# Kernel tuning notes

Measured on AMD Instinct MI355X. Metric: run time of the kernel, lower is better.

The kernel has to match this reference:

```python
import jax, jax.numpy as jnp
import numpy as np

B, S, E, H = 4, 2048, 1024, 16
K = 9           # number of boundaries per batch (K-1 = 8 passages)
DH = E // H


def make_relevance_mask(boundaries, relevance_scores, seq_len):
    """Vectorized equivalent of the Python-loop mask builder.

    boundaries: (B, K) int, sorted; boundaries[:,0] == q_end.
    relevance_scores: (B, K-1) float.
    Returns float mask (B, S, S) with values {0, 1, relevance}.
    """
    Bsz, Kb = boundaries.shape
    idx = jnp.arange(seq_len, dtype=boundaries.dtype)
    # pid[b, s] = j s.t. boundaries[b, j] <= s < boundaries[b, j+1]; -1 before b[0]
    pid = jax.vmap(lambda bb: jnp.searchsorted(bb, idx, side='right'))(boundaries) - 1  # (B,S)
    in_pass = (pid >= 0) & (pid < Kb - 1)  # inside some passage span
    rel_g = jnp.take_along_axis(relevance_scores, jnp.clip(pid, 0, Kb - 2), axis=1)  # (B,S)
    # query rows (pos < q_end): columns in passage j -> relevance[j], else 1
    col_val = jnp.where(in_pass, rel_g, 1.0)  # (B,S)
    qrow = idx[None, :] < boundaries[:, :1]   # (B,S)
    # non-query rows: 1 iff same passage block, else 0
    same = in_pass[:, :, None] & in_pass[:, None, :] & (pid[:, :, None] == pid[:, None, :])
    mask = jnp.where(qrow[:, :, None], col_val[:, None, :], jnp.where(same, 1.0, 0.0))
    return mask.astype(jnp.float32)


def setup_inputs() -> dict:
    key = jax.random.key(0)
    k1, k2, k3, k4, k5, k6, k7 = jax.random.split(key, 7)
    hidden_states = jax.random.normal(k1, (B, S, E), dtype=jnp.float32)
    relevance_scores = jax.random.uniform(k2, (B, K - 1), dtype=jnp.float32)
    passage_boundaries = jnp.sort(jax.random.randint(k3, (B, K), 0, S, dtype=jnp.int32), axis=1)
    in_proj_w = 0.02 * jax.random.normal(k4, (3 * E, E), dtype=jnp.float32)
    in_proj_b = jnp.zeros((3 * E,), dtype=jnp.float32)
    out_w = 0.02 * jax.random.normal(k5, (E, E), dtype=jnp.float32)
    out_b = jnp.zeros((E,), dtype=jnp.float32)
    return {
        'hidden_states': hidden_states,
        'relevance_scores': relevance_scores,
        'passage_boundaries': passage_boundaries,
        'in_proj_w': in_proj_w,
        'in_proj_b': in_proj_b,
        'out_w': out_w,
        'out_b': out_b,
    }


def reference(hidden_states, relevance_scores, passage_boundaries,
              in_proj_w, in_proj_b, out_w, out_b):
    Bsz, Sl, Em = hidden_states.shape
    mask = make_relevance_mask(passage_boundaries, relevance_scores, Sl)  # (B,S,S)
    qkv = hidden_states @ in_proj_w.T + in_proj_b              # (B,S,3E)
    q, k, v = jnp.split(qkv, 3, axis=-1)
    def heads(t):
        return t.reshape(Bsz, Sl, H, DH).transpose(0, 2, 1, 3)  # (B,H,S,Dh)
    q, k, v = heads(q), heads(k), heads(v)
    scale = 1.0 / jnp.sqrt(jnp.float32(DH))
    scores = jnp.einsum('bhqd,bhkd->bhqk', q * scale, k) + mask[:, None]  # float mask is ADDED
    attn = jax.nn.softmax(scores, axis=-1)
    out = jnp.einsum('bhqk,bhkd->bhqd', attn, v)
    out = out.transpose(0, 2, 1, 3).reshape(Bsz, Sl, Em)
    return out @ out_w.T + out_b
```

## Files before the change

kernel.cpp:

```cpp
#include <hip/hip_runtime.h>
#include <math.h>

#define Bsz 4
#define Sq  2048
#define Eq  1024
#define Hh  16
#define DHd 64
#define Kb  9
#define LOG2E 1.44269504088896340736f
#define NCLS 10

typedef _Float16 f16;
typedef __attribute__((ext_vector_type(8))) _Float16 fh8;
typedef __attribute__((ext_vector_type(4))) _Float16 fh4;
typedef __attribute__((ext_vector_type(2))) _Float16 fh2;
typedef __attribute__((ext_vector_type(4))) float fx4;
typedef __attribute__((ext_vector_type(16))) float fx16;
typedef __attribute__((ext_vector_type(4))) int i4;

#define SWZ(r, c) ((r) * 64 + ((c) ^ (((r) & 7) << 3)))

static __device__ __forceinline__ float fexp2(float x) {
#if __has_builtin(__builtin_amdgcn_exp2f)
  return __builtin_amdgcn_exp2f(x);
#else
  return __expf(x * 0.6931471805599453f);
#endif
}

__global__ void pid_kernel(const int* __restrict__ bnd, const float* __restrict__ rel,
                           int* __restrict__ pidr, float* __restrict__ lfTab) {
  int idx = blockIdx.x * blockDim.x + threadIdx.x;
  if (idx >= Bsz * Sq) return;
  int b = idx >> 11;
  int s = idx & (Sq - 1);
  int j = -1;
#pragma unroll
  for (int t = 0; t < Kb; ++t) {
    if (bnd[b * Kb + t] <= s) j = t;
  }
  pidr[idx] = j;
  bool inp = (j >= 0 && j < Kb - 1);
  float cv = inp ? rel[b * (Kb - 1) + j] : 1.0f;
  float* base = &lfTab[(size_t)b * NCLS * Sq + s];
  base[0] = cv * LOG2E;
#pragma unroll
  for (int c = 1; c < NCLS; ++c)
    base[c * Sq] = (inp && j == c - 1) ? LOG2E : 0.0f;
}

__global__ __launch_bounds__(256) void cvt_hs(const float* __restrict__ x,
                                              f16* __restrict__ xo) {
  int i = (blockIdx.x * blockDim.x + threadIdx.x) * 8;
  float4 a = *(const float4*)&x[i];
  float4 b = *(const float4*)&x[i + 4];
  fh8 o;
  o[0] = (f16)a.x; o[1] = (f16)a.y; o[2] = (f16)a.z; o[3] = (f16)a.w;
  o[4] = (f16)b.x; o[5] = (f16)b.y; o[6] = (f16)b.z; o[7] = (f16)b.w;
  *(fh8*)&xo[i] = o;
}

template <int MODE>
__global__ __launch_bounds__(256) void gemm_f16(
    const f16* __restrict__ A, const f16* __restrict__ Bh,
    const float* __restrict__ bias, float* __restrict__ Cp,
    int M, int N, int Kd,
    f16* __restrict__ qo, f16* __restrict__ ko, f16* __restrict__ vto) {
  __shared__ __align__(16) f16 Ash[2][128 * 64];
  __shared__ __align__(16) f16 Bsh[2][128 * 64];

  const int tid = threadIdx.x;
  const int lane = tid & 63, w = tid >> 6;
  const int wm = w >> 1, wn = w & 1;
  const int q16 = lane & 15, quad = lane >> 4;
  const int m_blk = blockIdx.y * 128, n_blk = blockIdx.x * 128;

  fx4 acc[4][4];
#pragma unroll
  for (int mt = 0; mt < 4; ++mt)
#pragma unroll
    for (int nt = 0; nt < 4; ++nt)
#pragma unroll
      for (int r = 0; r < 4; ++r) acc[mt][nt][r] = 0.f;

  const int rl = lane >> 3;
  const int bc = ((lane & 7) * 8) ^ (rl << 3);
  const f16* gA = A + (size_t)m_blk * Kd;
  const f16* gB = Bh + (size_t)n_blk * Kd;

  auto stage = [&](f16* dstA, f16* dstB, int k0) {
#pragma unroll
    for (int j = 0; j < 4; ++j) {
      const int r = w * 32 + j * 8;
      const f16* pa = gA + (size_t)(r + rl) * Kd + k0 + bc;
      const f16* pb = gB + (size_t)(r + rl) * Kd + k0 + bc;
#if __has_builtin(__builtin_amdgcn_global_load_lds)
      __builtin_amdgcn_global_load_lds(
          (const __attribute__((address_space(1))) void*)pa,
          (__attribute__((address_space(3))) void*)(dstA + r * 64), 16, 0, 0);
      __builtin_amdgcn_global_load_lds(
          (const __attribute__((address_space(1))) void*)pb,
          (__attribute__((address_space(3))) void*)(dstB + r * 64), 16, 0, 0);
#else
      *(fh8*)&dstA[r * 64 + lane * 8] = *(const fh8*)pa;
      *(fh8*)&dstB[r * 64 + lane * 8] = *(const fh8*)pb;
#endif
    }
  };

  stage(Ash[0], Bsh[0], 0);
  __syncthreads();

  for (int k0 = 0; k0 < Kd; k0 += 64) {
    const int c = (k0 >> 6) & 1;
    if (k0 + 64 < Kd) stage(Ash[c ^ 1], Bsh[c ^ 1], k0 + 64);

#pragma unroll
    for (int ks = 0; ks < 2; ++ks) {
      fh8 af[4], bfr[4];
#pragma unroll
      for (int mt = 0; mt < 4; ++mt)
        af[mt] = *(const fh8*)&Ash[c][SWZ(wm * 64 + mt * 16 + q16, ks * 32 + quad * 8)];
#pragma unroll
      for (int nt = 0; nt < 4; ++nt)
        bfr[nt] = *(const fh8*)&Bsh[c][SWZ(wn * 64 + nt * 16 + q16, ks * 32 + quad * 8)];
#pragma unroll
      for (int nt = 0; nt < 4; ++nt)
#pragma unroll
        for (int mt = 0; mt < 4; ++mt)
          acc[mt][nt] = __builtin_amdgcn_mfma_f32_16x16x32_f16(af[mt], bfr[nt], acc[mt][nt], 0, 0, 0);
    }
    __syncthreads();
  }

  float bsv[4];
#pragma unroll
  for (int nt = 0; nt < 4; ++nt) bsv[nt] = bias[n_blk + wn * 64 + nt * 16 + q16];

  if (MODE == 0) {
#pragma unroll
    for (int mt = 0; mt < 4; ++mt)
#pragma unroll
      for (int r = 0; r < 4; ++r) {
        int row = m_blk + wm * 64 + mt * 16 + quad * 4 + r;
#pragma unroll
        for (int nt = 0; nt < 4; ++nt) {
          int col = n_blk + wn * 64 + nt * 16 + q16;
          Cp[(size_t)row * N + col] = acc[mt][nt][r] + bsv[nt];
        }
      }
  } else {
    const int n0 = n_blk + wn * 64;
    const int which = n0 >> 10;
    const int hd = (n0 & 1023) >> 6;
    const float scale = (which == 0) ? 0.125f * LOG2E : 1.0f;
#pragma unroll
    for (int mt = 0; mt < 4; ++mt)
#pragma unroll
      for (int r = 0; r < 4; ++r) {
        int m = m_blk + wm * 64 + mt * 16 + quad * 4 + r;
        int b = m >> 11, s = m & (Sq - 1);
#pragma unroll
        for (int nt = 0; nt < 4; ++nt) {
          int d = nt * 16 + q16;
          float x = (acc[mt][nt][r] + bsv[nt]) * scale;
          if (which == 2) {
            vto[(((size_t)(b * Hh + hd)) * DHd + d) * Sq + s] = (f16)x;
          } else {
            f16* dst = (which == 0) ? qo : ko;
            dst[(((size_t)(b * Hh + hd)) * Sq + s) * DHd + d] = (f16)x;
          }
        }
      }
  }
}

__global__ __launch_bounds__(256, 2) void attn_v6(
    const f16* __restrict__ Qf, const f16* __restrict__ Kf,
    const f16* __restrict__ Vt, const int* __restrict__ pidr,
    const float* __restrict__ lfTab, f16* __restrict__ attf) {
  const int lin = blockIdx.x;
  const int orig = (lin & 7) * 128 + (lin >> 3);
  const int qb = orig & 15, hd = (orig >> 4) & 15, b = orig >> 8;
  const int bh = b * Hh + hd;
  const int tid = threadIdx.x;
  const int lane = tid & 63, w = tid >> 6;
  const int l31 = lane & 31, hi = lane >> 5;

  __shared__ __align__(16) f16 Ks[2][64 * 64];
  __shared__ __align__(16) f16 Vs[2][64 * 64];

  const size_t qkbase = (size_t)bh * Sq * DHd;
  const size_t vtbase = (size_t)bh * DHd * Sq;
  const int qrow = qb * 128 + w * 32 + l31;

  fh8 qf[4];
  {
    const f16* qp = &Qf[qkbase + (size_t)qrow * DHd + hi * 8];
#pragma unroll
    for (int ds = 0; ds < 4; ++ds) qf[ds] = *(const fh8*)&qp[ds * 16];
  }

  const int rq = pidr[b * Sq + qrow];
  const float* lfrow = &lfTab[((size_t)(b * NCLS + (rq + 1))) * Sq + 4 * hi];

  fh8 onesf;
#pragma unroll
  for (int j = 0; j < 8; ++j) onesf[j] = (l31 == 0) ? (f16)1.0f : (f16)0.0f;

  fx16 o_acc[2], lacc;
#pragma unroll
  for (int r = 0; r < 16; ++r) { o_acc[0][r] = 0.f; o_acc[1][r] = 0.f; lacc[r] = 0.f; }

  const int sr = tid >> 2, sc = (tid & 3) * 16;
  const int NT = Sq / 64;

  fh8 kc0, kc1, vc0, vc1;
  {
    const f16* gk = &Kf[qkbase + (size_t)sr * DHd + sc];
    kc0 = *(const fh8*)&gk[0]; kc1 = *(const fh8*)&gk[8];
    const f16* gv = &Vt[vtbase + (size_t)sr * Sq + sc];
    vc0 = *(const fh8*)&gv[0]; vc1 = *(const fh8*)&gv[8];
  }
  *(fh8*)&Ks[0][SWZ(sr, sc)]     = kc0;
  *(fh8*)&Ks[0][SWZ(sr, sc + 8)] = kc1;
  *(fh8*)&Vs[0][SWZ(sr, sc)]     = vc0;
  *(fh8*)&Vs[0][SWZ(sr, sc + 8)] = vc1;
  {
    const f16* gk = &Kf[qkbase + (size_t)(64 + sr) * DHd + sc];
    kc0 = *(const fh8*)&gk[0]; kc1 = *(const fh8*)&gk[8];
    const f16* gv = &Vt[vtbase + (size_t)sr * Sq + 64 + sc];
    vc0 = *(const fh8*)&gv[0]; vc1 = *(const fh8*)&gv[8];
  }
  __syncthreads();

  fx16 sacc0, sacc1;

  for (int kt = 0; kt < NT; ++kt) {
    const int c = kt & 1;

    {
      const float* lp = &lfrow[kt * 64];
#pragma unroll
      for (int g = 0; g < 4; ++g) {
        float4 a = *(const float4*)&lp[8 * g];
        sacc0[4 * g + 0] = a.x; sacc0[4 * g + 1] = a.y;
        sacc0[4 * g + 2] = a.z; sacc0[4 * g + 3] = a.w;
      }
    }

    if (kt + 1 < NT) {
      *(fh8*)&Ks[c ^ 1][SWZ(sr, sc)]     = kc0;
      *(fh8*)&Ks[c ^ 1][SWZ(sr, sc + 8)] = kc1;
      *(fh8*)&Vs[c ^ 1][SWZ(sr, sc)]     = vc0;
      *(fh8*)&Vs[c ^ 1][SWZ(sr, sc + 8)] = vc1;
      if (kt + 2 < NT) {
        const f16* gk = &Kf[qkbase + (size_t)((kt + 2) * 64 + sr) * DHd + sc];
        kc0 = *(const fh8*)&gk[0]; kc1 = *(const fh8*)&gk[8];
        const f16* gv = &Vt[vtbase + (size_t)sr * Sq + (kt + 2) * 64 + sc];
        vc0 = *(const fh8*)&gv[0]; vc1 = *(const fh8*)&gv[8];
      }
    }

    auto half = [&](fx16& sacc, int s, bool preload_next) {
      fh8 kfr[4];
#pragma unroll
      for (int ds = 0; ds < 4; ++ds)
        kfr[ds] = *(const fh8*)&Ks[c][SWZ(s * 32 + l31, ds * 16 + hi * 8)];
      __builtin_amdgcn_s_setprio(1);
#pragma unroll
      for (int ds = 0; ds < 4; ++ds)
        sacc = __builtin_amdgcn_mfma_f32_32x32x16_f16(kfr[ds], qf[ds], sacc, 0, 0, 0);
      __builtin_amdgcn_s_setprio(0);

      if (preload_next) {
        const float* lp = &lfrow[kt * 64 + 32];
#pragma unroll
        for (int g = 0; g < 4; ++g) {
          float4 a = *(const float4*)&lp[8 * g];
          sacc1[4 * g + 0] = a.x; sacc1[4 * g + 1] = a.y;
          sacc1[4 * g + 2] = a.z; sacc1[4 * g + 3] = a.w;
        }
      }

      int pk[8];
#pragma unroll
      for (int i = 0; i < 8; ++i) {
        fh2 h;
        h[0] = (f16)fexp2(sacc[2 * i]);
        h[1] = (f16)fexp2(sacc[2 * i + 1]);
        pk[i] = __builtin_bit_cast(int, h);
      }

      fh8 vfr[2][2];
#pragma unroll
      for (int dt = 0; dt < 2; ++dt)
#pragma unroll
        for (int kb = 0; kb < 2; ++kb)
          vfr[dt][kb] = *(const fh8*)&Vs[c][SWZ(dt * 32 + l31, s * 32 + kb * 16 + hi * 8)];

      __builtin_amdgcn_s_setprio(1);
#pragma unroll
      for (int kb = 0; kb < 2; ++kb) {
        int a01 = pk[4 * kb + 0], a23 = pk[4 * kb + 1];
        int a45 = pk[4 * kb + 2], a67 = pk[4 * kb + 3];
        i4 t;
#if __has_builtin(__builtin_amdgcn_permlane32_swap)
        auto s0 = __builtin_amdgcn_permlane32_swap(a01, a45, false, false);
        auto s1 = __builtin_amdgcn_permlane32_swap(a23, a67, false, false);
        t[0] = s0[0]; t[1] = s1[0]; t[2] = s0[1]; t[3] = s1[1];
#else
        int x01 = __shfl_xor(a01, 32), x23 = __shfl_xor(a23, 32);
        int x45 = __shfl_xor(a45, 32), x67 = __shfl_xor(a67, 32);
        t[0] = hi ? x45 : a01; t[1] = hi ? x67 : a23;
        t[2] = hi ? a45 : x01; t[3] = hi ? a67 : x23;
#endif
        fh8 pf = __builtin_bit_cast(fh8, t);
        lacc = __builtin_amdgcn_mfma_f32_32x32x16_f16(onesf, pf, lacc, 0, 0, 0);
        o_acc[0] = __builtin_amdgcn_mfma_f32_32x32x16_f16(vfr[0][kb], pf, o_acc[0], 0, 0, 0);
        o_acc[1] = __builtin_amdgcn_mfma_f32_32x32x16_f16(vfr[1][kb], pf, o_acc[1], 0, 0, 0);
      }
      __builtin_amdgcn_s_setprio(0);
    };

    half(sacc0, 0, true);
    half(sacc1, 1, false);

    if (kt + 1 < NT) __syncthreads();
  }

  float l = __shfl(lacc[0], l31);
  float inv = 1.0f / l;
  size_t obase = ((size_t)(b * Sq + qrow)) * Eq + hd * 64 + 4 * hi;
#pragma unroll
  for (int dt = 0; dt < 2; ++dt)
#pragma unroll
    for (int g = 0; g < 4; ++g) {
      fh4 o4;
#pragma unroll
      for (int j = 0; j < 4; ++j) o4[j] = (f16)(o_acc[dt][4 * g + j] * inv);
      *(fh4*)&attf[obase + dt * 32 + 8 * g] = o4;
    }
}

extern "C" void kernel_launch(void* const* d_in, const int* in_sizes, int n_in,
                              void* d_out, int out_size, void* d_ws, size_t ws_size,
                              hipStream_t stream) {
  const float* hs = (const float*)d_in[0];
  const float* rel = (const float*)d_in[1];
  const int* bnd = (const int*)d_in[2];
  const float* wi = (const float*)d_in[3];
  const float* bi = (const float*)d_in[4];
  const float* wo = (const float*)d_in[5];
  const float* bo = (const float*)d_in[6];
  float* out = (float*)d_out;

  const size_t NQ = (size_t)Bsz * Hh * Sq * DHd;
  char* p = (char*)d_ws;
  f16* qf = (f16*)p;   p += NQ * 2;
  f16* kf = (f16*)p;   p += NQ * 2;
  f16* vt = (f16*)p;   p += NQ * 2;
  f16* hsf = (f16*)p;  p += NQ * 2;
  f16* attf = (f16*)p; p += NQ * 2;
  f16* wif = (f16*)p;  p += (size_t)3 * Eq * Eq * 2;
  f16* wof = (f16*)p;  p += (size_t)Eq * Eq * 2;
  int* pidr = (int*)p; p += Bsz * Sq * 4;
  float* lfTab = (float*)p;

  hipLaunchKernelGGL(pid_kernel, dim3((Bsz * Sq + 255) / 256), dim3(256), 0, stream,
                     bnd, rel, pidr, lfTab);
  hipLaunchKernelGGL(cvt_hs, dim3((int)(NQ / 2048)), dim3(256), 0, stream, hs, hsf);
  hipLaunchKernelGGL(cvt_hs, dim3(3 * Eq * Eq / 2048), dim3(256), 0, stream, wi, wif);
  hipLaunchKernelGGL(cvt_hs, dim3(Eq * Eq / 2048), dim3(256), 0, stream, wo, wof);
  hipLaunchKernelGGL((gemm_f16<1>), dim3(24, 64), dim3(256), 0, stream,
                     hsf, wif, bi, (float*)nullptr, Bsz * Sq, 3 * Eq, Eq,
                     qf, kf, vt);
  hipLaunchKernelGGL(attn_v6, dim3(16 * 16 * 4), dim3(256), 0, stream,
                     qf, kf, vt, pidr, lfTab, attf);
  hipLaunchKernelGGL((gemm_f16<0>), dim3(8, 64), dim3(256), 0, stream,
                     attf, wof, bo, out, Bsz * Sq, Eq, Eq,
                     nullptr, nullptr, nullptr);
}
```

Measured before the change: 313.7 us.

## Fuse prep kernels into one launch and single-buffer GEMM shared tiles

Merges the three fp16 conversion kernels and the passage-id/mask-table kernel into a single prep launch, dispatching on block index, to cut launch count. The GEMM switches from double-buffered LDS staging to a single buffer with sync before and after each load, halving LDS use so more blocks can be resident. The trade-off is that global-to-LDS loads no longer overlap with MFMA work inside a block, so it relies on occupancy to hide that latency.

```diff
diff --git a/kernel.cpp b/kernel.cpp
--- a/kernel.cpp
+++ b/kernel.cpp
@@ -28,36 +28,46 @@
 #endif
 }
 
-__global__ void pid_kernel(const int* __restrict__ bnd, const float* __restrict__ rel,
-                           int* __restrict__ pidr, float* __restrict__ lfTab) {
-  int idx = blockIdx.x * blockDim.x + threadIdx.x;
-  if (idx >= Bsz * Sq) return;
-  int b = idx >> 11;
-  int s = idx & (Sq - 1);
-  int j = -1;
-#pragma unroll
-  for (int t = 0; t < Kb; ++t) {
-    if (bnd[b * Kb + t] <= s) j = t;
-  }
-  pidr[idx] = j;
-  bool inp = (j >= 0 && j < Kb - 1);
-  float cv = inp ? rel[b * (Kb - 1) + j] : 1.0f;
-  float* base = &lfTab[(size_t)b * NCLS * Sq + s];
-  base[0] = cv * LOG2E;
-#pragma unroll
-  for (int c = 1; c < NCLS; ++c)
-    base[c * Sq] = (inp && j == c - 1) ? LOG2E : 0.0f;
-}
-
-__global__ __launch_bounds__(256) void cvt_hs(const float* __restrict__ x,
-                                              f16* __restrict__ xo) {
-  int i = (blockIdx.x * blockDim.x + threadIdx.x) * 8;
-  float4 a = *(const float4*)&x[i];
-  float4 b = *(const float4*)&x[i + 4];
-  fh8 o;
-  o[0] = (f16)a.x; o[1] = (f16)a.y; o[2] = (f16)a.z; o[3] = (f16)a.w;
-  o[4] = (f16)b.x; o[5] = (f16)b.y; o[6] = (f16)b.z; o[7] = (f16)b.w;
-  *(fh8*)&xo[i] = o;
+__global__ __launch_bounds__(256) void prep(
+    const float* __restrict__ hs, f16* __restrict__ hsf,
+    const float* __restrict__ wi, f16* __restrict__ wif,
+    const float* __restrict__ wo, f16* __restrict__ wof,
+    const int* __restrict__ bnd, const float* __restrict__ rel,
+    int* __restrict__ pidr, float* __restrict__ lfTab) {
+  const int bid = blockIdx.x;
+  if (bid < 6144) {
+    const float* src;
+    f16* dst;
+    int off;
+    if (bid < 4096)      { src = hs; dst = hsf; off = bid; }
+    else if (bid < 5632) { src = wi; dst = wif; off = bid - 4096; }
+    else                 { src = wo; dst = wof; off = bid - 5632; }
+    int i = (off * 256 + threadIdx.x) * 8;
+    float4 a = *(const float4*)&src[i];
+    float4 b = *(const float4*)&src[i + 4];
+    fh8 o;
+    o[0] = (f16)a.x; o[1] = (f16)a.y; o[2] = (f16)a.z; o[3] = (f16)a.w;
+    o[4] = (f16)b.x; o[5] = (f16)b.y; o[6] = (f16)b.z; o[7] = (f16)b.w;
+    *(fh8*)&dst[i] = o;
+  } else {
+    int idx = (bid - 6144) * 256 + threadIdx.x;
+    if (idx >= Bsz * Sq) return;
+    int b = idx >> 11;
+    int s = idx & (Sq - 1);
+    int j = -1;
+#pragma unroll
+    for (int t = 0; t < Kb; ++t) {
+      if (bnd[b * Kb + t] <= s) j = t;
+    }
+    pidr[idx] = j;
+    bool inp = (j >= 0 && j < Kb - 1);
+    float cv = inp ? rel[b * (Kb - 1) + j] : 1.0f;
+    float* base = &lfTab[(size_t)b * NCLS * Sq + s];
+    base[0] = cv * LOG2E;
+#pragma unroll
+    for (int c = 1; c < NCLS; ++c)
+      base[c * Sq] = (inp && j == c - 1) ? LOG2E : 0.0f;
+  }
 }
 
 template <int MODE>
@@ -66,8 +76,8 @@
     const float* __restrict__ bias, float* __restrict__ Cp,
     int M, int N, int Kd,
     f16* __restrict__ qo, f16* __restrict__ ko, f16* __restrict__ vto) {
-  __shared__ __align__(16) f16 Ash[2][128 * 64];
-  __shared__ __align__(16) f16 Bsh[2][128 * 64];
+  __shared__ __align__(16) f16 Ash[128 * 64];
+  __shared__ __align__(16) f16 Bsh[128 * 64];
 
   const int tid = threadIdx.x;
   const int lane = tid & 63, w = tid >> 6;
@@ -88,7 +98,8 @@
   const f16* gA = A + (size_t)m_blk * Kd;
   const f16* gB = Bh + (size_t)n_blk * Kd;
 
-  auto stage = [&](f16* dstA, f16* dstB, int k0) {
+  for (int k0 = 0; k0 < Kd; k0 += 64) {
+    __syncthreads();
 #pragma unroll
     for (int j = 0; j < 4; ++j) {
       const int r = w * 32 + j * 8;
@@ -97,40 +108,32 @@
 #if __has_builtin(__builtin_amdgcn_global_load_lds)
       __builtin_amdgcn_global_load_lds(
           (const __attribute__((address_space(1))) void*)pa,
-          (__attribute__((address_space(3))) void*)(dstA + r * 64), 16, 0, 0);
+          (__attribute__((address_space(3))) void*)(Ash + r * 64), 16, 0, 0);
       __builtin_amdgcn_global_load_lds(
           (const __attribute__((address_space(1))) void*)pb,
-          (__attribute__((address_space(3))) void*)(dstB + r * 64), 16, 0, 0);
+          (__attribute__((address_space(3))) void*)(Bsh + r * 64), 16, 0, 0);
 #else
-      *(fh8*)&dstA[r * 64 + lane * 8] = *(const fh8*)pa;
-      *(fh8*)&dstB[r * 64 + lane * 8] = *(const fh8*)pb;
+      *(fh8*)&Ash[r * 64 + lane * 8] = *(const fh8*)pa;
+      *(fh8*)&Bsh[r * 64 + lane * 8] = *(const fh8*)pb;
 #endif
     }
-  };
-
-  stage(Ash[0], Bsh[0], 0);
-  __syncthreads();
-
-  for (int k0 = 0; k0 < Kd; k0 += 64) {
-    const int c = (k0 >> 6) & 1;
-    if (k0 + 64 < Kd) stage(Ash[c ^ 1], Bsh[c ^ 1], k0 + 64);
+    __syncthreads();
 
 #pragma unroll
     for (int ks = 0; ks < 2; ++ks) {
       fh8 af[4], bfr[4];
 #pragma unroll
       for (int mt = 0; mt < 4; ++mt)
-        af[mt] = *(const fh8*)&Ash[c][SWZ(wm * 64 + mt * 16 + q16, ks * 32 + quad * 8)];
+        af[mt] = *(const fh8*)&Ash[SWZ(wm * 64 + mt * 16 + q16, ks * 32 + quad * 8)];
 #pragma unroll
       for (int nt = 0; nt < 4; ++nt)
-        bfr[nt] = *(const fh8*)&Bsh[c][SWZ(wn * 64 + nt * 16 + q16, ks * 32 + quad * 8)];
+        bfr[nt] = *(const fh8*)&Bsh[SWZ(wn * 64 + nt * 16 + q16, ks * 32 + quad * 8)];
 #pragma unroll
       for (int nt = 0; nt < 4; ++nt)
 #pragma unroll
         for (int mt = 0; mt < 4; ++mt)
           acc[mt][nt] = __builtin_amdgcn_mfma_f32_16x16x32_f16(af[mt], bfr[nt], acc[mt][nt], 0, 0, 0);
     }
-    __syncthreads();
   }
 
   float bsv[4];
@@ -367,11 +370,8 @@
   int* pidr = (int*)p; p += Bsz * Sq * 4;
   float* lfTab = (float*)p;
 
-  hipLaunchKernelGGL(pid_kernel, dim3((Bsz * Sq + 255) / 256), dim3(256), 0, stream,
-                     bnd, rel, pidr, lfTab);
-  hipLaunchKernelGGL(cvt_hs, dim3((int)(NQ / 2048)), dim3(256), 0, stream, hs, hsf);
-  hipLaunchKernelGGL(cvt_hs, dim3(3 * Eq * Eq / 2048), dim3(256), 0, stream, wi, wif);
-  hipLaunchKernelGGL(cvt_hs, dim3(Eq * Eq / 2048), dim3(256), 0, stream, wo, wof);
+  hipLaunchKernelGGL(prep, dim3(6176), dim3(256), 0, stream,
+                     hs, hsf, wi, wif, wo, wof, bnd, rel, pidr, lfTab);
   hipLaunchKernelGGL((gemm_f16<1>), dim3(24, 64), dim3(256), 0, stream,
                      hsf, wif, bi, (float*)nullptr, Bsz * Sq, 3 * Eq, Eq,
                      qf, kf, vt);
```

After: 308.1 us. Within noise of the previous version (-1.8%).
